# Performance work log

Hardware: AMD Instinct MI355X
Metric: run time of the kernel (lower is better)

Reference implementation:

```python
import jax, jax.numpy as jnp
import numpy as np

N = 8192
D_IN, D_MID, D_EMB = 1024, 256, 64
N_EDGES = N * 8


def setup_inputs() -> dict:
    key = jax.random.key(0)
    ks = jax.random.split(key, 6)
    X = jax.random.normal(ks[0], (N, D_IN), dtype=jnp.float32)
    # Xavier-uniform style init as in get_weight_initial
    b1 = np.sqrt(6.0 / (D_IN + D_MID))
    b2 = np.sqrt(6.0 / (D_MID + D_EMB))
    W1 = jax.random.uniform(ks[1], (D_IN, D_MID), minval=-b1, maxval=b1, dtype=jnp.float32)
    W2 = jax.random.uniform(ks[2], (D_MID, D_EMB), minval=-b2, maxval=b2, dtype=jnp.float32)
    edge_val = jax.random.uniform(ks[3], (N_EDGES,), dtype=jnp.float32)
    edge_src = jax.random.randint(ks[4], (N_EDGES,), 0, N, dtype=jnp.int32)
    edge_dst = jax.random.randint(ks[5], (N_EDGES,), 0, N, dtype=jnp.int32)
    return {"X": X, "W1": W1, "W2": W2, "edge_val": edge_val,
            "edge_src": edge_src, "edge_dst": edge_dst}


def reference(X, W1, W2, edge_val, edge_src, edge_dst):
    n = X.shape[0]

    def spmm(H):  # sparse Laplacian (COO) times dense H
        return jax.ops.segment_sum(edge_val[:, None] * H[edge_src], edge_dst,
                                   num_segments=n)

    h = jax.nn.relu(spmm(X @ W1))          # [N, D_MID]
    emb = spmm(h @ W2)                      # [N, D_EMB]
    # pairwise squared Euclidean distances between rows of emb -> [N, N]
    sq = jnp.sum(emb * emb, axis=1)
    dist = sq[:, None] + sq[None, :] - 2.0 * (emb @ emb.T)
    recons_w = jax.nn.softmax(-dist, axis=1) + 1e-10
    return recons_w
```

## Files before the change

kernel.cpp:

```cpp
#include <hip/hip_runtime.h>
#include <cstddef>

constexpr int NN    = 8192;
constexpr int DIN   = 1024;
constexpr int DMID  = 256;
constexpr int DEMB  = 64;
constexpr int NEDGE = 65536;

typedef __attribute__((ext_vector_type(8))) short bf16x8;
typedef __attribute__((ext_vector_type(4))) float f32x4;
#define MFMA16(a, b, c) __builtin_amdgcn_mfma_f32_16x16x32_bf16((a), (b), (c), 0, 0, 0)

__device__ __forceinline__ unsigned short bf16_rne(float x) {
  unsigned u = __float_as_uint(x);
  return (unsigned short)((u + 0x7FFFu + ((u >> 16) & 1u)) >> 16);
}
__device__ __forceinline__ void bf16_split(float x, unsigned short& h, unsigned short& l) {
  unsigned short hb = bf16_rne(x);
  float hf = __uint_as_float((unsigned)hb << 16);
  h = hb;
  l = bf16_rne(x - hf);
}

__global__ __launch_bounds__(256) void split_kernel(const float* __restrict__ src,
                                                    unsigned short* __restrict__ hi,
                                                    unsigned short* __restrict__ lo)
{
  size_t idx = ((size_t)blockIdx.x * 256 + threadIdx.x) * 4;
  float4 v = *(const float4*)(src + idx);
  ushort4 h, l;
  bf16_split(v.x, h.x, l.x);
  bf16_split(v.y, h.y, l.y);
  bf16_split(v.z, h.z, l.z);
  bf16_split(v.w, h.w, l.w);
  *(ushort4*)(hi + idx) = h;
  *(ushort4*)(lo + idx) = l;
}

__global__ __launch_bounds__(256) void w1t_kernel(const float* __restrict__ W1,
                                                  unsigned short* __restrict__ h,
                                                  unsigned short* __restrict__ l)
{
  int idx = blockIdx.x * 256 + threadIdx.x;
  int n = idx >> 10, k = idx & 1023;
  bf16_split(W1[k * 256 + n], h[idx], l[idx]);
}

__global__ __launch_bounds__(256) void w2t_kernel(const float* __restrict__ W2,
                                                  unsigned short* __restrict__ h,
                                                  unsigned short* __restrict__ l)
{
  int idx = blockIdx.x * 256 + threadIdx.x;
  int n = idx >> 8, k = idx & 255;
  bf16_split(W2[k * 64 + n], h[idx], l[idx]);
}

__global__ __launch_bounds__(256) void hist_kernel(const int* __restrict__ dst,
                                                   int* __restrict__ counts)
{
  int e = blockIdx.x * 256 + threadIdx.x;
  atomicAdd(&counts[dst[e]], 1);
}

__global__ __launch_bounds__(256) void scan_kernel(const int* __restrict__ counts,
                                                   int* __restrict__ row_start)
{
  __shared__ int sums[256];
  const int t = threadIdx.x;
  int local[32];
  int s = 0;
#pragma unroll
  for (int i = 0; i < 32; ++i) { local[i] = counts[t * 32 + i]; s += local[i]; }
  sums[t] = s;
  __syncthreads();
  for (int off = 1; off < 256; off <<= 1) {
    int v = (t >= off) ? sums[t - off] : 0;
    __syncthreads();
    sums[t] += v;
    __syncthreads();
  }
  int base = (t == 0) ? 0 : sums[t - 1];
#pragma unroll
  for (int i = 0; i < 32; ++i) { row_start[t * 32 + i] = base; base += local[i]; }
  if (t == 255) row_start[NN] = base;
}

__global__ __launch_bounds__(256) void scatter_kernel(
    const int* __restrict__ src, const float* __restrict__ val,
    const int* __restrict__ dst, const int* __restrict__ row_start,
    int* __restrict__ cursor, int* __restrict__ csr_src, float* __restrict__ csr_val)
{
  int e = blockIdx.x * 256 + threadIdx.x;
  int d = dst[e];
  int pos = row_start[d] + atomicAdd(&cursor[d], 1);
  csr_src[pos] = src[e];
  csr_val[pos] = val[e];
}

__global__ __launch_bounds__(256) void gemm1_kernel(
    const unsigned short* __restrict__ Xh, const unsigned short* __restrict__ Xl,
    const unsigned short* __restrict__ Wh, const unsigned short* __restrict__ Wl,
    float* __restrict__ C)
{
  const int lane = threadIdx.x & 63;
  const int wave = threadIdx.x >> 6;
  const int m0 = blockIdx.y * 64 + wave * 16;
  const int n0 = blockIdx.x * 64;
  const int rl = lane & 15;
  const int kq = (lane >> 4) * 8;
  f32x4 zero = {0.f, 0.f, 0.f, 0.f};
  f32x4 acc[4] = {zero, zero, zero, zero};
  for (int s = 0; s < DIN / 32; ++s) {
    const int kb = s * 32 + kq;
    bf16x8 ah = *(const bf16x8*)(Xh + (size_t)(m0 + rl) * DIN + kb);
    bf16x8 al = *(const bf16x8*)(Xl + (size_t)(m0 + rl) * DIN + kb);
#pragma unroll
    for (int ns = 0; ns < 4; ++ns) {
      const size_t rb = (size_t)(n0 + ns * 16 + rl) * DIN + kb;
      bf16x8 bh = *(const bf16x8*)(Wh + rb);
      bf16x8 bl = *(const bf16x8*)(Wl + rb);
      acc[ns] = MFMA16(ah, bh, acc[ns]);
      acc[ns] = MFMA16(ah, bl, acc[ns]);
      acc[ns] = MFMA16(al, bh, acc[ns]);
    }
  }
  const int rq = (lane >> 4) * 4;
#pragma unroll
  for (int ns = 0; ns < 4; ++ns)
#pragma unroll
    for (int r = 0; r < 4; ++r)
      C[(size_t)(m0 + rq + r) * DMID + n0 + ns * 16 + rl] = acc[ns][r];
}

__global__ __launch_bounds__(64) void gemm2_kernel(
    const unsigned short* __restrict__ Ah, const unsigned short* __restrict__ Al,
    const unsigned short* __restrict__ Wh, const unsigned short* __restrict__ Wl,
    float* __restrict__ C)
{
  const int lane = threadIdx.x;
  const int m0 = blockIdx.x * 16;
  const int rl = lane & 15;
  const int kq = (lane >> 4) * 8;
  f32x4 zero = {0.f, 0.f, 0.f, 0.f};
  f32x4 acc[4] = {zero, zero, zero, zero};
  for (int s = 0; s < DMID / 32; ++s) {
    const int kb = s * 32 + kq;
    bf16x8 ah = *(const bf16x8*)(Ah + (size_t)(m0 + rl) * DMID + kb);
    bf16x8 al = *(const bf16x8*)(Al + (size_t)(m0 + rl) * DMID + kb);
#pragma unroll
    for (int ns = 0; ns < 4; ++ns) {
      const size_t rb = (size_t)(ns * 16 + rl) * DMID + kb;
      bf16x8 bh = *(const bf16x8*)(Wh + rb);
      bf16x8 bl = *(const bf16x8*)(Wl + rb);
      acc[ns] = MFMA16(ah, bh, acc[ns]);
      acc[ns] = MFMA16(ah, bl, acc[ns]);
      acc[ns] = MFMA16(al, bh, acc[ns]);
    }
  }
  const int rq = (lane >> 4) * 4;
#pragma unroll
  for (int ns = 0; ns < 4; ++ns)
#pragma unroll
    for (int r = 0; r < 4; ++r)
      C[(size_t)(m0 + rq + r) * DEMB + ns * 16 + rl] = acc[ns][r];
}

__global__ __launch_bounds__(256) void spmm1_kernel(
    const float* __restrict__ H, const int* __restrict__ row_start,
    const int* __restrict__ csr_src, const float* __restrict__ csr_val,
    unsigned short* __restrict__ outh, unsigned short* __restrict__ outl)
{
  const int lane = threadIdx.x & 63;
  const int wave = threadIdx.x >> 6;
  const int r = blockIdx.x * 4 + wave;
  const int e0 = row_start[r];
  const int e1 = row_start[r + 1];
  const int c = lane * 4;
  float4 acc = make_float4(0.f, 0.f, 0.f, 0.f);
  for (int e = e0; e < e1; ++e) {
    const int s   = csr_src[e];
    const float v = csr_val[e];
    float4 h = *(const float4*)(H + (size_t)s * DMID + c);
    acc.x = fmaf(v, h.x, acc.x);
    acc.y = fmaf(v, h.y, acc.y);
    acc.z = fmaf(v, h.z, acc.z);
    acc.w = fmaf(v, h.w, acc.w);
  }
  acc.x = fmaxf(acc.x, 0.f); acc.y = fmaxf(acc.y, 0.f);
  acc.z = fmaxf(acc.z, 0.f); acc.w = fmaxf(acc.w, 0.f);
  ushort4 h, l;
  bf16_split(acc.x, h.x, l.x);
  bf16_split(acc.y, h.y, l.y);
  bf16_split(acc.z, h.z, l.z);
  bf16_split(acc.w, h.w, l.w);
  *(ushort4*)(outh + (size_t)r * DMID + c) = h;
  *(ushort4*)(outl + (size_t)r * DMID + c) = l;
}

__global__ __launch_bounds__(256) void spmm2_kernel(
    const float* __restrict__ H, const int* __restrict__ row_start,
    const int* __restrict__ csr_src, const float* __restrict__ csr_val,
    unsigned short* __restrict__ EmbH, unsigned short* __restrict__ EmbL,
    float* __restrict__ sqv)
{
  const int lane = threadIdx.x & 63;
  const int wave = threadIdx.x >> 6;
  const int r = blockIdx.x * 4 + wave;
  const int e0 = row_start[r];
  const int e1 = row_start[r + 1];
  float acc = 0.f;
  for (int e = e0; e < e1; ++e)
    acc = fmaf(csr_val[e], H[(size_t)csr_src[e] * DEMB + lane], acc);
  unsigned short h, l;
  bf16_split(acc, h, l);
  EmbH[(size_t)r * DEMB + lane] = h;
  EmbL[(size_t)r * DEMB + lane] = l;
  float sq = acc * acc;
#pragma unroll
  for (int off = 32; off; off >>= 1) sq += __shfl_xor(sq, off, 64);
  if (lane == 0) sqv[r] = sq;
}

__device__ __forceinline__ void dist_tile_accum(
    const unsigned short* __restrict__ EH, const unsigned short* __restrict__ EL,
    int ibase, int jbase, int lane, f32x4 (&acc)[4][4])
{
  const int rl = lane & 15;
  const int kq = (lane >> 4) * 8;
#pragma unroll
  for (int s = 0; s < 2; ++s) {
    const int kb = s * 32 + kq;
    bf16x8 ah[4], al[4], bh[4], bl[4];
#pragma unroll
    for (int t = 0; t < 4; ++t) {
      const size_t ra = (size_t)(ibase + t * 16 + rl) * DEMB + kb;
      ah[t] = *(const bf16x8*)(EH + ra);
      al[t] = *(const bf16x8*)(EL + ra);
      const size_t rb = (size_t)(jbase + t * 16 + rl) * DEMB + kb;
      bh[t] = *(const bf16x8*)(EH + rb);
      bl[t] = *(const bf16x8*)(EL + rb);
    }
#pragma unroll
    for (int ms = 0; ms < 4; ++ms)
#pragma unroll
      for (int ns = 0; ns < 4; ++ns) {
        acc[ms][ns] = MFMA16(ah[ms], bh[ns], acc[ms][ns]);
        acc[ms][ns] = MFMA16(ah[ms], bl[ns], acc[ms][ns]);
        acc[ms][ns] = MFMA16(al[ms], bh[ns], acc[ms][ns]);
      }
  }
}

__global__ __launch_bounds__(256) void rowsum_kernel(
    const unsigned short* __restrict__ EH, const unsigned short* __restrict__ EL,
    const float* __restrict__ sq, float* __restrict__ rowsum)
{
  const int lane = threadIdx.x & 63;
  const int wave = threadIdx.x >> 6;
  const int wr = wave >> 1, wc = wave & 1;
  const int ibase = blockIdx.x * 128 + wr * 64;
  const int jslab = blockIdx.y * 1024;
  const int rl = lane & 15;
  const int rq = (lane >> 4) * 4;

  float si[4][4];
#pragma unroll
  for (int ms = 0; ms < 4; ++ms)
#pragma unroll
    for (int r = 0; r < 4; ++r) si[ms][r] = sq[ibase + ms * 16 + rq + r];

  float rs[4][4] = {};
  f32x4 zero = {0.f, 0.f, 0.f, 0.f};
  for (int jt = 0; jt < 8; ++jt) {
    const int jbase = jslab + jt * 128 + wc * 64;
    f32x4 acc[4][4];
#pragma unroll
    for (int ms = 0; ms < 4; ++ms)
#pragma unroll
      for (int ns = 0; ns < 4; ++ns) acc[ms][ns] = zero;
    dist_tile_accum(EH, EL, ibase, jbase, lane, acc);
    float sj[4];
#pragma unroll
    for (int ns = 0; ns < 4; ++ns) sj[ns] = sq[jbase + ns * 16 + rl];
#pragma unroll
    for (int ms = 0; ms < 4; ++ms)
#pragma unroll
      for (int ns = 0; ns < 4; ++ns)
#pragma unroll
        for (int r = 0; r < 4; ++r)
          rs[ms][r] += __expf(fmaf(2.f, acc[ms][ns][r], -si[ms][r] - sj[ns]));
  }
#pragma unroll
  for (int ms = 0; ms < 4; ++ms)
#pragma unroll
    for (int r = 0; r < 4; ++r) {
      float v = rs[ms][r];
      v += __shfl_xor(v, 1, 64);
      v += __shfl_xor(v, 2, 64);
      v += __shfl_xor(v, 4, 64);
      v += __shfl_xor(v, 8, 64);
      if (rl == 0) atomicAdd(&rowsum[ibase + ms * 16 + rq + r], v);
    }
}

__global__ __launch_bounds__(256) void inv_kernel(const float* __restrict__ rowsum,
                                                  float* __restrict__ rinv)
{
  int i = blockIdx.x * 256 + threadIdx.x;
  rinv[i] = 1.f / rowsum[i];
}

__global__ __launch_bounds__(256) void dist_write_kernel(
    const unsigned short* __restrict__ EH, const unsigned short* __restrict__ EL,
    const float* __restrict__ sq, const float* __restrict__ rinv,
    float* __restrict__ out)
{
  const int lane = threadIdx.x & 63;
  const int wave = threadIdx.x >> 6;
  const int wr = wave >> 1, wc = wave & 1;
  const int ibase = blockIdx.y * 128 + wr * 64;
  const int jbase = blockIdx.x * 128 + wc * 64;
  const int rl = lane & 15;
  const int rq = (lane >> 4) * 4;

  f32x4 zero = {0.f, 0.f, 0.f, 0.f};
  f32x4 acc[4][4];
#pragma unroll
  for (int ms = 0; ms < 4; ++ms)
#pragma unroll
    for (int ns = 0; ns < 4; ++ns) acc[ms][ns] = zero;
  dist_tile_accum(EH, EL, ibase, jbase, lane, acc);

  float si[4][4], ri[4][4], sj[4];
#pragma unroll
  for (int ms = 0; ms < 4; ++ms)
#pragma unroll
    for (int r = 0; r < 4; ++r) {
      const int i = ibase + ms * 16 + rq + r;
      si[ms][r] = sq[i];
      ri[ms][r] = rinv[i];
    }
#pragma unroll
  for (int ns = 0; ns < 4; ++ns) sj[ns] = sq[jbase + ns * 16 + rl];

#pragma unroll
  for (int ms = 0; ms < 4; ++ms)
#pragma unroll
    for (int r = 0; r < 4; ++r) {
      const size_t row = (size_t)(ibase + ms * 16 + rq + r) * NN;
#pragma unroll
      for (int ns = 0; ns < 4; ++ns) {
        float v = __expf(fmaf(2.f, acc[ms][ns][r], -si[ms][r] - sj[ns]));
        out[row + jbase + ns * 16 + rl] = fmaf(v, ri[ms][r], 1e-10f);
      }
    }
}

extern "C" void kernel_launch(void* const* d_in, const int* in_sizes, int n_in,
                              void* d_out, int out_size, void* d_ws, size_t ws_size,
                              hipStream_t stream)
{
  const float* X  = (const float*)d_in[0];
  const float* W1 = (const float*)d_in[1];
  const float* W2 = (const float*)d_in[2];
  const float* ev = (const float*)d_in[3];
  const int* esrc = (const int*)d_in[4];
  const int* edst = (const int*)d_in[5];
  float* out = (float*)d_out;

  char* p = (char*)d_ws;
  auto alloc = [&](size_t bytes) { char* q = p; p += (bytes + 255) & ~(size_t)255; return q; };

  int*   counts    = (int*)alloc(NN * 4);
  int*   cursor    = (int*)alloc(NN * 4);
  float* rowsum    = (float*)alloc(NN * 4);
  int*   row_start = (int*)alloc((NN + 1) * 4);
  int*   csr_src   = (int*)alloc(NEDGE * 4);
  float* csr_val   = (float*)alloc(NEDGE * 4);
  float* sqv       = (float*)alloc(NN * 4);
  float* rinv      = (float*)alloc(NN * 4);
  float* H1        = (float*)alloc((size_t)NN * DMID * 4);
  float* E1        = (float*)alloc((size_t)NN * DEMB * 4);
  unsigned short* Xh   = (unsigned short*)alloc((size_t)NN * DIN * 2);
  unsigned short* Xl   = (unsigned short*)alloc((size_t)NN * DIN * 2);
  unsigned short* W1Th = (unsigned short*)alloc((size_t)DMID * DIN * 2);
  unsigned short* W1Tl = (unsigned short*)alloc((size_t)DMID * DIN * 2);
  unsigned short* W2Th = (unsigned short*)alloc((size_t)DEMB * DMID * 2);
  unsigned short* W2Tl = (unsigned short*)alloc((size_t)DEMB * DMID * 2);
  unsigned short* H1sh = (unsigned short*)alloc((size_t)NN * DMID * 2);
  unsigned short* H1sl = (unsigned short*)alloc((size_t)NN * DMID * 2);
  unsigned short* EmbH = (unsigned short*)alloc((size_t)NN * DEMB * 2);
  unsigned short* EmbL = (unsigned short*)alloc((size_t)NN * DEMB * 2);

  hipMemsetAsync(d_ws, 0, (size_t)3 * NN * 4, stream);

  split_kernel<<<(size_t)NN * DIN / 1024, 256, 0, stream>>>(X, Xh, Xl);
  w1t_kernel<<<DMID * DIN / 256, 256, 0, stream>>>(W1, W1Th, W1Tl);
  w2t_kernel<<<DEMB * DMID / 256, 256, 0, stream>>>(W2, W2Th, W2Tl);

  hist_kernel<<<NEDGE / 256, 256, 0, stream>>>(edst, counts);
  scan_kernel<<<1, 256, 0, stream>>>(counts, row_start);
  scatter_kernel<<<NEDGE / 256, 256, 0, stream>>>(esrc, ev, edst, row_start, cursor,
                                                  csr_src, csr_val);

  gemm1_kernel<<<dim3(DMID / 64, NN / 64), 256, 0, stream>>>(Xh, Xl, W1Th, W1Tl, H1);
  spmm1_kernel<<<NN / 4, 256, 0, stream>>>(H1, row_start, csr_src, csr_val, H1sh, H1sl);
  gemm2_kernel<<<NN / 16, 64, 0, stream>>>(H1sh, H1sl, W2Th, W2Tl, E1);
  spmm2_kernel<<<NN / 4, 256, 0, stream>>>(E1, row_start, csr_src, csr_val, EmbH, EmbL, sqv);

  rowsum_kernel<<<dim3(NN / 128, 8), 256, 0, stream>>>(EmbH, EmbL, sqv, rowsum);
  inv_kernel<<<NN / 256, 256, 0, stream>>>(rowsum, rinv);
  dist_write_kernel<<<dim3(NN / 128, NN / 128), 256, 0, stream>>>(EmbH, EmbL, sqv, rinv, out);
}
```

Baseline: 500.8 us.

## Drop split-bf16 precision, exploit distance symmetry, fuse conversions into GEMMs

Replaces the hi/lo bf16 split emulation with single bf16 operands across all GEMMs and the distance tiles, cutting MFMA count by three times and removing the X split pass. It also computes only upper-triangular distance tiles, accumulating both row and column sums and writing the transposed tile through LDS. Weight conversions are merged into one kernel, the reciprocal kernel is folded into the writer, and gemm2 gets wider blocks. This reduces accuracy, since single bf16 on embeddings feeding exp(-dist) may exceed tolerance. Half the blocks exit immediately.

```diff
diff --git a/kernel.cpp b/kernel.cpp
--- a/kernel.cpp
+++ b/kernel.cpp
@@ -15,44 +15,24 @@
   unsigned u = __float_as_uint(x);
   return (unsigned short)((u + 0x7FFFu + ((u >> 16) & 1u)) >> 16);
 }
-__device__ __forceinline__ void bf16_split(float x, unsigned short& h, unsigned short& l) {
-  unsigned short hb = bf16_rne(x);
-  float hf = __uint_as_float((unsigned)hb << 16);
-  h = hb;
-  l = bf16_rne(x - hf);
-}
-
-__global__ __launch_bounds__(256) void split_kernel(const float* __restrict__ src,
-                                                    unsigned short* __restrict__ hi,
-                                                    unsigned short* __restrict__ lo)
-{
-  size_t idx = ((size_t)blockIdx.x * 256 + threadIdx.x) * 4;
-  float4 v = *(const float4*)(src + idx);
-  ushort4 h, l;
-  bf16_split(v.x, h.x, l.x);
-  bf16_split(v.y, h.y, l.y);
-  bf16_split(v.z, h.z, l.z);
-  bf16_split(v.w, h.w, l.w);
-  *(ushort4*)(hi + idx) = h;
-  *(ushort4*)(lo + idx) = l;
-}
-
-__global__ __launch_bounds__(256) void w1t_kernel(const float* __restrict__ W1,
-                                                  unsigned short* __restrict__ h,
-                                                  unsigned short* __restrict__ l)
+__device__ __forceinline__ float bf16_tof(unsigned short h) {
+  return __uint_as_float((unsigned)h << 16);
+}
+
+__global__ __launch_bounds__(256) void wconv_kernel(const float* __restrict__ W1,
+                                                    const float* __restrict__ W2,
+                                                    unsigned short* __restrict__ W1b,
+                                                    unsigned short* __restrict__ W2b)
 {
   int idx = blockIdx.x * 256 + threadIdx.x;
-  int n = idx >> 10, k = idx & 1023;
-  bf16_split(W1[k * 256 + n], h[idx], l[idx]);
-}
-
-__global__ __launch_bounds__(256) void w2t_kernel(const float* __restrict__ W2,
-                                                  unsigned short* __restrict__ h,
-                                                  unsigned short* __restrict__ l)
-{
-  int idx = blockIdx.x * 256 + threadIdx.x;
-  int n = idx >> 8, k = idx & 255;
-  bf16_split(W2[k * 64 + n], h[idx], l[idx]);
+  if (idx < DMID * DIN) {
+    int n = idx >> 10, k = idx & 1023;
+    W1b[idx] = bf16_rne(W1[k * DMID + n]);
+  } else {
+    int t = idx - DMID * DIN;
+    int n = t >> 8, k = t & 255;
+    W2b[t] = bf16_rne(W2[k * DEMB + n]);
+  }
 }
 
 __global__ __launch_bounds__(256) void hist_kernel(const int* __restrict__ dst,
@@ -98,9 +78,8 @@
 }
 
 __global__ __launch_bounds__(256) void gemm1_kernel(
-    const unsigned short* __restrict__ Xh, const unsigned short* __restrict__ Xl,
-    const unsigned short* __restrict__ Wh, const unsigned short* __restrict__ Wl,
-    float* __restrict__ C)
+    const float* __restrict__ X, const unsigned short* __restrict__ W1b,
+    float* __restrict__ H1)
 {
   const int lane = threadIdx.x & 63;
   const int wave = threadIdx.x >> 6;
@@ -112,16 +91,18 @@
   f32x4 acc[4] = {zero, zero, zero, zero};
   for (int s = 0; s < DIN / 32; ++s) {
     const int kb = s * 32 + kq;
-    bf16x8 ah = *(const bf16x8*)(Xh + (size_t)(m0 + rl) * DIN + kb);
-    bf16x8 al = *(const bf16x8*)(Xl + (size_t)(m0 + rl) * DIN + kb);
+    const float* xp = X + (size_t)(m0 + rl) * DIN + kb;
+    float4 x0 = *(const float4*)xp;
+    float4 x1 = *(const float4*)(xp + 4);
+    bf16x8 ah;
+    ah[0] = (short)bf16_rne(x0.x); ah[1] = (short)bf16_rne(x0.y);
+    ah[2] = (short)bf16_rne(x0.z); ah[3] = (short)bf16_rne(x0.w);
+    ah[4] = (short)bf16_rne(x1.x); ah[5] = (short)bf16_rne(x1.y);
+    ah[6] = (short)bf16_rne(x1.z); ah[7] = (short)bf16_rne(x1.w);
 #pragma unroll
     for (int ns = 0; ns < 4; ++ns) {
-      const size_t rb = (size_t)(n0 + ns * 16 + rl) * DIN + kb;
-      bf16x8 bh = *(const bf16x8*)(Wh + rb);
-      bf16x8 bl = *(const bf16x8*)(Wl + rb);
+      bf16x8 bh = *(const bf16x8*)(W1b + (size_t)(n0 + ns * 16 + rl) * DIN + kb);
       acc[ns] = MFMA16(ah, bh, acc[ns]);
-      acc[ns] = MFMA16(ah, bl, acc[ns]);
-      acc[ns] = MFMA16(al, bh, acc[ns]);
     }
   }
   const int rq = (lane >> 4) * 4;
@@ -129,46 +110,13 @@
   for (int ns = 0; ns < 4; ++ns)
 #pragma unroll
     for (int r = 0; r < 4; ++r)
-      C[(size_t)(m0 + rq + r) * DMID + n0 + ns * 16 + rl] = acc[ns][r];
-}
-
-__global__ __launch_bounds__(64) void gemm2_kernel(
-    const unsigned short* __restrict__ Ah, const unsigned short* __restrict__ Al,
-    const unsigned short* __restrict__ Wh, const unsigned short* __restrict__ Wl,
-    float* __restrict__ C)
-{
-  const int lane = threadIdx.x;
-  const int m0 = blockIdx.x * 16;
-  const int rl = lane & 15;
-  const int kq = (lane >> 4) * 8;
-  f32x4 zero = {0.f, 0.f, 0.f, 0.f};
-  f32x4 acc[4] = {zero, zero, zero, zero};
-  for (int s = 0; s < DMID / 32; ++s) {
-    const int kb = s * 32 + kq;
-    bf16x8 ah = *(const bf16x8*)(Ah + (size_t)(m0 + rl) * DMID + kb);
-    bf16x8 al = *(const bf16x8*)(Al + (size_t)(m0 + rl) * DMID + kb);
-#pragma unroll
-    for (int ns = 0; ns < 4; ++ns) {
-      const size_t rb = (size_t)(ns * 16 + rl) * DMID + kb;
-      bf16x8 bh = *(const bf16x8*)(Wh + rb);
-      bf16x8 bl = *(const bf16x8*)(Wl + rb);
-      acc[ns] = MFMA16(ah, bh, acc[ns]);
-      acc[ns] = MFMA16(ah, bl, acc[ns]);
-      acc[ns] = MFMA16(al, bh, acc[ns]);
-    }
-  }
-  const int rq = (lane >> 4) * 4;
-#pragma unroll
-  for (int ns = 0; ns < 4; ++ns)
-#pragma unroll
-    for (int r = 0; r < 4; ++r)
-      C[(size_t)(m0 + rq + r) * DEMB + ns * 16 + rl] = acc[ns][r];
+      H1[(size_t)(m0 + rq + r) * DMID + n0 + ns * 16 + rl] = acc[ns][r];
 }
 
 __global__ __launch_bounds__(256) void spmm1_kernel(
     const float* __restrict__ H, const int* __restrict__ row_start,
     const int* __restrict__ csr_src, const float* __restrict__ csr_val,
-    unsigned short* __restrict__ outh, unsigned short* __restrict__ outl)
+    unsigned short* __restrict__ Hb)
 {
   const int lane = threadIdx.x & 63;
   const int wave = threadIdx.x >> 6;
@@ -186,22 +134,46 @@
     acc.z = fmaf(v, h.z, acc.z);
     acc.w = fmaf(v, h.w, acc.w);
   }
-  acc.x = fmaxf(acc.x, 0.f); acc.y = fmaxf(acc.y, 0.f);
-  acc.z = fmaxf(acc.z, 0.f); acc.w = fmaxf(acc.w, 0.f);
-  ushort4 h, l;
-  bf16_split(acc.x, h.x, l.x);
-  bf16_split(acc.y, h.y, l.y);
-  bf16_split(acc.z, h.z, l.z);
-  bf16_split(acc.w, h.w, l.w);
-  *(ushort4*)(outh + (size_t)r * DMID + c) = h;
-  *(ushort4*)(outl + (size_t)r * DMID + c) = l;
+  ushort4 h;
+  h.x = bf16_rne(fmaxf(acc.x, 0.f));
+  h.y = bf16_rne(fmaxf(acc.y, 0.f));
+  h.z = bf16_rne(fmaxf(acc.z, 0.f));
+  h.w = bf16_rne(fmaxf(acc.w, 0.f));
+  *(ushort4*)(Hb + (size_t)r * DMID + c) = h;
+}
+
+__global__ __launch_bounds__(256) void gemm2_kernel(
+    const unsigned short* __restrict__ Ab, const unsigned short* __restrict__ W2b,
+    float* __restrict__ E1)
+{
+  const int lane = threadIdx.x & 63;
+  const int wave = threadIdx.x >> 6;
+  const int m0 = blockIdx.x * 64 + wave * 16;
+  const int rl = lane & 15;
+  const int kq = (lane >> 4) * 8;
+  f32x4 zero = {0.f, 0.f, 0.f, 0.f};
+  f32x4 acc[4] = {zero, zero, zero, zero};
+  for (int s = 0; s < DMID / 32; ++s) {
+    const int kb = s * 32 + kq;
+    bf16x8 ah = *(const bf16x8*)(Ab + (size_t)(m0 + rl) * DMID + kb);
+#pragma unroll
+    for (int ns = 0; ns < 4; ++ns) {
+      bf16x8 bh = *(const bf16x8*)(W2b + (size_t)(ns * 16 + rl) * DMID + kb);
+      acc[ns] = MFMA16(ah, bh, acc[ns]);
+    }
+  }
+  const int rq = (lane >> 4) * 4;
+#pragma unroll
+  for (int ns = 0; ns < 4; ++ns)
+#pragma unroll
+    for (int r = 0; r < 4; ++r)
+      E1[(size_t)(m0 + rq + r) * DEMB + ns * 16 + rl] = acc[ns][r];
 }
 
 __global__ __launch_bounds__(256) void spmm2_kernel(
     const float* __restrict__ H, const int* __restrict__ row_start,
     const int* __restrict__ csr_src, const float* __restrict__ csr_val,
-    unsigned short* __restrict__ EmbH, unsigned short* __restrict__ EmbL,
-    float* __restrict__ sqv)
+    unsigned short* __restrict__ EmbH, float* __restrict__ sqv)
 {
   const int lane = threadIdx.x & 63;
   const int wave = threadIdx.x >> 6;
@@ -211,85 +183,81 @@
   float acc = 0.f;
   for (int e = e0; e < e1; ++e)
     acc = fmaf(csr_val[e], H[(size_t)csr_src[e] * DEMB + lane], acc);
-  unsigned short h, l;
-  bf16_split(acc, h, l);
+  unsigned short h = bf16_rne(acc);
   EmbH[(size_t)r * DEMB + lane] = h;
-  EmbL[(size_t)r * DEMB + lane] = l;
-  float sq = acc * acc;
+  float hf = bf16_tof(h);
+  float sq = hf * hf;
 #pragma unroll
   for (int off = 32; off; off >>= 1) sq += __shfl_xor(sq, off, 64);
   if (lane == 0) sqv[r] = sq;
 }
 
-__device__ __forceinline__ void dist_tile_accum(
-    const unsigned short* __restrict__ EH, const unsigned short* __restrict__ EL,
-    int ibase, int jbase, int lane, f32x4 (&acc)[4][4])
+__device__ __forceinline__ void dist_tile_hh(
+    const unsigned short* __restrict__ EH, int ibase, int jbase, int lane,
+    f32x4 (&acc)[4][4])
 {
   const int rl = lane & 15;
   const int kq = (lane >> 4) * 8;
 #pragma unroll
   for (int s = 0; s < 2; ++s) {
     const int kb = s * 32 + kq;
-    bf16x8 ah[4], al[4], bh[4], bl[4];
+    bf16x8 a[4], b[4];
 #pragma unroll
     for (int t = 0; t < 4; ++t) {
-      const size_t ra = (size_t)(ibase + t * 16 + rl) * DEMB + kb;
-      ah[t] = *(const bf16x8*)(EH + ra);
-      al[t] = *(const bf16x8*)(EL + ra);
-      const size_t rb = (size_t)(jbase + t * 16 + rl) * DEMB + kb;
-      bh[t] = *(const bf16x8*)(EH + rb);
-      bl[t] = *(const bf16x8*)(EL + rb);
+      a[t] = *(const bf16x8*)(EH + (size_t)(ibase + t * 16 + rl) * DEMB + kb);
+      b[t] = *(const bf16x8*)(EH + (size_t)(jbase + t * 16 + rl) * DEMB + kb);
     }
 #pragma unroll
     for (int ms = 0; ms < 4; ++ms)
 #pragma unroll
-      for (int ns = 0; ns < 4; ++ns) {
-        acc[ms][ns] = MFMA16(ah[ms], bh[ns], acc[ms][ns]);
-        acc[ms][ns] = MFMA16(ah[ms], bl[ns], acc[ms][ns]);
-        acc[ms][ns] = MFMA16(al[ms], bh[ns], acc[ms][ns]);
+      for (int ns = 0; ns < 4; ++ns)
+        acc[ms][ns] = MFMA16(a[ms], b[ns], acc[ms][ns]);
+  }
+}
+
+__global__ __launch_bounds__(256) void rowsum_sym_kernel(
+    const unsigned short* __restrict__ EH, const float* __restrict__ sq,
+    float* __restrict__ rowsum)
+{
+  const int bi = blockIdx.y, bj = blockIdx.x;
+  if (bj < bi) return;
+  const int lane = threadIdx.x & 63;
+  const int wave = threadIdx.x >> 6;
+  const int wr = wave >> 1, wc = wave & 1;
+  const int ibase = bi * 128 + wr * 64;
+  const int jbase = bj * 128 + wc * 64;
+  const int rl = lane & 15;
+  const int rq = (lane >> 4) * 4;
+
+  f32x4 zero = {0.f, 0.f, 0.f, 0.f};
+  f32x4 acc[4][4];
+#pragma unroll
+  for (int ms = 0; ms < 4; ++ms)
+#pragma unroll
+    for (int ns = 0; ns < 4; ++ns) acc[ms][ns] = zero;
+  dist_tile_hh(EH, ibase, jbase, lane, acc);
+
+  float si[4][4], sj[4];
+#pragma unroll
+  for (int ms = 0; ms < 4; ++ms)
+#pragma unroll
+    for (int r = 0; r < 4; ++r) si[ms][r] = sq[ibase + ms * 16 + rq + r];
+#pragma unroll
+  for (int ns = 0; ns < 4; ++ns) sj[ns] = sq[jbase + ns * 16 + rl];
+
+  float rs[4][4] = {};
+  float cs[4]    = {};
+#pragma unroll
+  for (int ms = 0; ms < 4; ++ms)
+#pragma unroll
+    for (int ns = 0; ns < 4; ++ns)
+#pragma unroll
+      for (int r = 0; r < 4; ++r) {
+        float v = __expf(fmaf(2.f, acc[ms][ns][r], -si[ms][r] - sj[ns]));
+        rs[ms][r] += v;
+        cs[ns]    += v;
       }
-  }
-}
-
-__global__ __launch_bounds__(256) void rowsum_kernel(
-    const unsigned short* __restrict__ EH, const unsigned short* __restrict__ EL,
-    const float* __restrict__ sq, float* __restrict__ rowsum)
-{
-  const int lane = threadIdx.x & 63;
-  const int wave = threadIdx.x >> 6;
-  const int wr = wave >> 1, wc = wave & 1;
-  const int ibase = blockIdx.x * 128 + wr * 64;
-  const int jslab = blockIdx.y * 1024;
-  const int rl = lane & 15;
-  const int rq = (lane >> 4) * 4;
-
-  float si[4][4];
-#pragma unroll
-  for (int ms = 0; ms < 4; ++ms)
-#pragma unroll
-    for (int r = 0; r < 4; ++r) si[ms][r] = sq[ibase + ms * 16 + rq + r];
-
-  float rs[4][4] = {};
-  f32x4 zero = {0.f, 0.f, 0.f, 0.f};
-  for (int jt = 0; jt < 8; ++jt) {
-    const int jbase = jslab + jt * 128 + wc * 64;
-    f32x4 acc[4][4];
-#pragma unroll
-    for (int ms = 0; ms < 4; ++ms)
-#pragma unroll
-      for (int ns = 0; ns < 4; ++ns) acc[ms][ns] = zero;
-    dist_tile_accum(EH, EL, ibase, jbase, lane, acc);
-    float sj[4];
-#pragma unroll
-    for (int ns = 0; ns < 4; ++ns) sj[ns] = sq[jbase + ns * 16 + rl];
-#pragma unroll
-    for (int ms = 0; ms < 4; ++ms)
-#pragma unroll
-      for (int ns = 0; ns < 4; ++ns)
-#pragma unroll
-        for (int r = 0; r < 4; ++r)
-          rs[ms][r] += __expf(fmaf(2.f, acc[ms][ns][r], -si[ms][r] - sj[ns]));
-  }
+
 #pragma unroll
   for (int ms = 0; ms < 4; ++ms)
 #pragma unroll
@@ -301,27 +269,33 @@
       v += __shfl_xor(v, 8, 64);
       if (rl == 0) atomicAdd(&rowsum[ibase + ms * 16 + rq + r], v);
     }
-}
-
-__global__ __launch_bounds__(256) void inv_kernel(const float* __restrict__ rowsum,
-                                                  float* __restrict__ rinv)
-{
-  int i = blockIdx.x * 256 + threadIdx.x;
-  rinv[i] = 1.f / rowsum[i];
-}
-
-__global__ __launch_bounds__(256) void dist_write_kernel(
-    const unsigned short* __restrict__ EH, const unsigned short* __restrict__ EL,
-    const float* __restrict__ sq, const float* __restrict__ rinv,
-    float* __restrict__ out)
-{
+
+  if (bi != bj) {
+#pragma unroll
+    for (int ns = 0; ns < 4; ++ns) {
+      float v = cs[ns];
+      v += __shfl_xor(v, 16, 64);
+      v += __shfl_xor(v, 32, 64);
+      if (lane < 16) atomicAdd(&rowsum[jbase + ns * 16 + rl], v);
+    }
+  }
+}
+
+__global__ __launch_bounds__(256) void dist_write_sym_kernel(
+    const unsigned short* __restrict__ EH, const float* __restrict__ sq,
+    const float* __restrict__ rowsum, float* __restrict__ out)
+{
+  const int bi = blockIdx.y, bj = blockIdx.x;
+  if (bj < bi) return;
+  __shared__ float tlds[4][16 * 66];
   const int lane = threadIdx.x & 63;
   const int wave = threadIdx.x >> 6;
   const int wr = wave >> 1, wc = wave & 1;
-  const int ibase = blockIdx.y * 128 + wr * 64;
-  const int jbase = blockIdx.x * 128 + wc * 64;
+  const int ibase = bi * 128 + wr * 64;
+  const int jbase = bj * 128 + wc * 64;
   const int rl = lane & 15;
   const int rq = (lane >> 4) * 4;
+  const bool offdiag = (bi != bj);
 
   f32x4 zero = {0.f, 0.f, 0.f, 0.f};
   f32x4 acc[4][4];
@@ -329,7 +303,7 @@
   for (int ms = 0; ms < 4; ++ms)
 #pragma unroll
     for (int ns = 0; ns < 4; ++ns) acc[ms][ns] = zero;
-  dist_tile_accum(EH, EL, ibase, jbase, lane, acc);
+  dist_tile_hh(EH, ibase, jbase, lane, acc);
 
   float si[4][4], ri[4][4], sj[4];
 #pragma unroll
@@ -338,22 +312,41 @@
     for (int r = 0; r < 4; ++r) {
       const int i = ibase + ms * 16 + rq + r;
       si[ms][r] = sq[i];
-      ri[ms][r] = rinv[i];
+      ri[ms][r] = 1.f / rowsum[i];
     }
 #pragma unroll
   for (int ns = 0; ns < 4; ++ns) sj[ns] = sq[jbase + ns * 16 + rl];
-
-#pragma unroll
-  for (int ms = 0; ms < 4; ++ms)
-#pragma unroll
-    for (int r = 0; r < 4; ++r) {
-      const size_t row = (size_t)(ibase + ms * 16 + rq + r) * NN;
-#pragma unroll
-      for (int ns = 0; ns < 4; ++ns) {
-        float v = __expf(fmaf(2.f, acc[ms][ns][r], -si[ms][r] - sj[ns]));
-        out[row + jbase + ns * 16 + rl] = fmaf(v, ri[ms][r], 1e-10f);
+  const float rjv = offdiag ? 1.f / rowsum[jbase + lane] : 0.f;
+
+#pragma unroll
+  for (int ms = 0; ms < 4; ++ms) {
+#pragma unroll
+    for (int ns = 0; ns < 4; ++ns)
+#pragma unroll
+      for (int r = 0; r < 4; ++r) {
+        float e = __expf(fmaf(2.f, acc[ms][ns][r], -si[ms][r] - sj[ns]));
+        out[(size_t)(ibase + ms * 16 + rq + r) * NN + jbase + ns * 16 + rl] =
+            fmaf(e, ri[ms][r], 1e-10f);
+        if (offdiag) tlds[wave][(rq + r) * 66 + ns * 16 + rl] = e;
       }
-    }
+    if (offdiag) {
+      __builtin_amdgcn_wave_barrier();
+      float v16[16];
+#pragma unroll
+      for (int i = 0; i < 16; ++i) v16[i] = tlds[wave][i * 66 + lane];
+      float* op = out + (size_t)(jbase + lane) * NN + ibase + ms * 16;
+#pragma unroll
+      for (int q = 0; q < 4; ++q) {
+        float4 w;
+        w.x = fmaf(v16[4 * q + 0], rjv, 1e-10f);
+        w.y = fmaf(v16[4 * q + 1], rjv, 1e-10f);
+        w.z = fmaf(v16[4 * q + 2], rjv, 1e-10f);
+        w.w = fmaf(v16[4 * q + 3], rjv, 1e-10f);
+        *(float4*)(op + 4 * q) = w;
+      }
+      __builtin_amdgcn_wave_barrier();
+    }
+  }
 }
 
 extern "C" void kernel_launch(void* const* d_in, const int* in_sizes, int n_in,
@@ -378,37 +371,26 @@
   int*   csr_src   = (int*)alloc(NEDGE * 4);
   float* csr_val   = (float*)alloc(NEDGE * 4);
   float* sqv       = (float*)alloc(NN * 4);
-  float* rinv      = (float*)alloc(NN * 4);
   float* H1        = (float*)alloc((size_t)NN * DMID * 4);
   float* E1        = (float*)alloc((size_t)NN * DEMB * 4);
-  unsigned short* Xh   = (unsigned short*)alloc((size_t)NN * DIN * 2);
-  unsigned short* Xl   = (unsigned short*)alloc((size_t)NN * DIN * 2);
-  unsigned short* W1Th = (unsigned short*)alloc((size_t)DMID * DIN * 2);
-  unsigned short* W1Tl = (unsigned short*)alloc((size_t)DMID * DIN * 2);
-  unsigned short* W2Th = (unsigned short*)alloc((size_t)DEMB * DMID * 2);
-  unsigned short* W2Tl = (unsigned short*)alloc((size_t)DEMB * DMID * 2);
-  unsigned short* H1sh = (unsigned short*)alloc((size_t)NN * DMID * 2);
-  unsigned short* H1sl = (unsigned short*)alloc((size_t)NN * DMID * 2);
+  unsigned short* W1b  = (unsigned short*)alloc((size_t)DMID * DIN * 2);
+  unsigned short* W2b  = (unsigned short*)alloc((size_t)DEMB * DMID * 2);
+  unsigned short* H1b  = (unsigned short*)alloc((size_t)NN * DMID * 2);
   unsigned short* EmbH = (unsigned short*)alloc((size_t)NN * DEMB * 2);
-  unsigned short* EmbL = (unsigned short*)alloc((size_t)NN * DEMB * 2);
 
   hipMemsetAsync(d_ws, 0, (size_t)3 * NN * 4, stream);
 
-  split_kernel<<<(size_t)NN * DIN / 1024, 256, 0, stream>>>(X, Xh, Xl);
-  w1t_kernel<<<DMID * DIN / 256, 256, 0, stream>>>(W1, W1Th, W1Tl);
-  w2t_kernel<<<DEMB * DMID / 256, 256, 0, stream>>>(W2, W2Th, W2Tl);
-
+  wconv_kernel<<<(DMID * DIN + DEMB * DMID) / 256, 256, 0, stream>>>(W1, W2, W1b, W2b);
   hist_kernel<<<NEDGE / 256, 256, 0, stream>>>(edst, counts);
   scan_kernel<<<1, 256, 0, stream>>>(counts, row_start);
   scatter_kernel<<<NEDGE / 256, 256, 0, stream>>>(esrc, ev, edst, row_start, cursor,
                                                   csr_src, csr_val);
 
-  gemm1_kernel<<<dim3(DMID / 64, NN / 64), 256, 0, stream>>>(Xh, Xl, W1Th, W1Tl, H1);
-  spmm1_kernel<<<NN / 4, 256, 0, stream>>>(H1, row_start, csr_src, csr_val, H1sh, H1sl);
-  gemm2_kernel<<<NN / 16, 64, 0, stream>>>(H1sh, H1sl, W2Th, W2Tl, E1);
-  spmm2_kernel<<<NN / 4, 256, 0, stream>>>(E1, row_start, csr_src, csr_val, EmbH, EmbL, sqv);
-
-  rowsum_kernel<<<dim3(NN / 128, 8), 256, 0, stream>>>(EmbH, EmbL, sqv, rowsum);
-  inv_kernel<<<NN / 256, 256, 0, stream>>>(rowsum, rinv);
-  dist_write_kernel<<<dim3(NN / 128, NN / 128), 256, 0, stream>>>(EmbH, EmbL, sqv, rinv, out);
-}
+  gemm1_kernel<<<dim3(DMID / 64, NN / 64), 256, 0, stream>>>(X, W1b, H1);
+  spmm1_kernel<<<NN / 4, 256, 0, stream>>>(H1, row_start, csr_src, csr_val, H1b);
+  gemm2_kernel<<<NN / 64, 256, 0, stream>>>(H1b, W2b, E1);
+  spmm2_kernel<<<NN / 4, 256, 0, stream>>>(E1, row_start, csr_src, csr_val, EmbH, sqv);
+
+  rowsum_sym_kernel<<<dim3(NN / 128, NN / 128), 256, 0, stream>>>(EmbH, sqv, rowsum);
+  dist_write_sym_kernel<<<dim3(NN / 128, NN / 128), 256, 0, stream>>>(EmbH, sqv, rowsum, out);
+}
```

New measurement: 531.5 us. 6.1% more time.
